# Kernel optimization log

Hardware: AMD Instinct MI355X
Metric: run time of the kernel (lower is better)

The kernel has to match this reference:

```python
import jax, jax.numpy as jnp
import numpy as np

N_SEQ, MAX_LEN, H_DIM, N_CHAR = 8, 4096, 1024, 256


def setup_inputs() -> dict:
    key = jax.random.key(0)
    ks = jax.random.split(key, 10)
    n_char_ev = 32768
    L, E = 12, 16384
    char_i_seq = jax.random.randint(ks[0], (n_char_ev,), 0, N_SEQ)
    char_i_pos = jax.random.randint(ks[1], (n_char_ev,), 0, MAX_LEN)
    char_ids = jax.random.randint(ks[2], (n_char_ev,), 0, N_CHAR)
    grp_i_seq = jax.random.randint(ks[3], (L, E), 0, N_SEQ)
    grp_i_first = jax.random.randint(ks[4], (L, E), 0, MAX_LEN)
    grp_i_second = jax.random.randint(ks[5], (L, E), 0, MAX_LEN)
    grp_i_pos = jax.random.randint(ks[6], (L, E), 0, MAX_LEN)
    # Learned params: embedding table (std = 1/sqrt(h_dim)) and composer Linear(2h -> h)
    emb_char = jax.random.normal(ks[7], (N_CHAR, H_DIM), dtype=jnp.float32) * (1.0 / H_DIM ** 0.5)
    W = jax.random.normal(ks[8], (2 * H_DIM, H_DIM), dtype=jnp.float32) * (1.0 / (2 * H_DIM) ** 0.5)
    b = jnp.zeros((H_DIM,), dtype=jnp.float32)
    return {"char_i_seq": char_i_seq, "char_i_pos": char_i_pos, "char_ids": char_ids,
            "grp_i_seq": grp_i_seq, "grp_i_first": grp_i_first, "grp_i_second": grp_i_second,
            "grp_i_pos": grp_i_pos, "emb_char": emb_char, "W": W, "b": b}


def reference(char_i_seq, char_i_pos, char_ids, grp_i_seq, grp_i_first,
              grp_i_second, grp_i_pos, emb_char, W, b):
    # h_frag: [n_seq, max_len, h_dim]
    h = jnp.zeros((N_SEQ, MAX_LEN, H_DIM), dtype=emb_char.dtype)
    # Leaf characters: embedding lookup + scatter-add
    h = h.at[char_i_seq, char_i_pos].add(emb_char[char_ids])

    def composer(left, right):
        # tanh(Linear(concat(left, right))) : [E, 2h] @ [2h, h] -> [E, h]
        return jnp.tanh(jnp.concatenate([left, right], axis=-1) @ W + b)

    def level_step(h, idx):
        i_seq, i_first, i_second, i_pos = idx
        out = composer(h[i_seq, i_first], h[i_seq, i_second])  # gather -> compose
        return h.at[i_seq, i_pos].add(out), None                # scatter-add

    h, _ = jax.lax.scan(level_step, h, (grp_i_seq, grp_i_first, grp_i_second, grp_i_pos))
    h = h.at[:, 0].set(0.0)  # h_frag[:, 0].fill_(0)
    return h
```

## Files before the change

kernel.cpp:

```cpp
#include <hip/hip_runtime.h>

#define NS 8
#define ML 4096
#define HD 1024
#define K2 2048
#define NEV 32768
#define NLEV 12
#define NE 16384
#define NSLOT (NS * ML)
#define CAP 8
#define BK 64
#define NT (K2 / BK)
#define LDS_BYTES 131072

typedef __attribute__((ext_vector_type(8))) short bf16x8;
typedef __attribute__((ext_vector_type(4))) float f32x4;

typedef __attribute__((address_space(1))) const void cvoid_g;
typedef __attribute__((address_space(3))) void void_l;

static __device__ __forceinline__ void load_lds_16(const void* g, void* l) {
    __builtin_amdgcn_global_load_lds((cvoid_g*)g, (void_l*)l, 16, 0, 0);
}

static __device__ __forceinline__ unsigned short f2bf(float f) {
    unsigned u = __float_as_uint(f);
    unsigned r = (u + 0x7fffu + ((u >> 16) & 1u)) >> 16;
    return (unsigned short)r;
}

static __device__ __forceinline__ float fast_tanh(float x) {
    return 1.0f - 2.0f / (__expf(2.0f * x) + 1.0f);
}

__global__ void wt_kernel(const float* __restrict__ W, unsigned short* __restrict__ WbT) {
    __shared__ unsigned short tile[64][65];
    const int t = threadIdx.x;
    const int k0 = blockIdx.x * 64;
    const int n0 = blockIdx.y * 64;
#pragma unroll
    for (int i = 0; i < 16; i++) {
        int idx = i * 256 + t;
        int r = idx >> 6, c = idx & 63;
        tile[r][c] = f2bf(W[(size_t)(k0 + r) * HD + n0 + c]);
    }
    __syncthreads();
#pragma unroll
    for (int i = 0; i < 16; i++) {
        int idx = i * 256 + t;
        int r = idx >> 6, c = idx & 63;
        WbT[(size_t)(n0 + r) * K2 + k0 + c] = tile[c][r];
    }
}

__global__ void char_ticket(const int* __restrict__ cseq, const int* __restrict__ cpos,
                            int* __restrict__ counts, int* __restrict__ ticket,
                            int* __restrict__ evlist) {
    const int e = blockIdx.x * 256 + threadIdx.x;
    if (e >= NEV) return;
    const int slot = cseq[e] * ML + cpos[e];
    const int t = atomicAdd(&counts[slot], 1);
    ticket[e] = t;
    if (t < CAP) evlist[slot * CAP + t] = e;
}

__global__ void char_slot_sum(const int* __restrict__ counts, const int* __restrict__ evlist,
                              const int* __restrict__ cid, const float* __restrict__ emb,
                              float* __restrict__ h) {
    const int slot = blockIdx.x;
    const int t = threadIdx.x;
    int n = counts[slot];
    if (n > CAP) n = CAP;
    float4 acc = {0.f, 0.f, 0.f, 0.f};
    for (int i = 0; i < n; i++) {
        const int e = evlist[slot * CAP + i];
        const int id = cid[e];
        const float4 v = ((const float4*)(emb + (size_t)id * HD))[t];
        acc.x += v.x; acc.y += v.y; acc.z += v.z; acc.w += v.w;
    }
    ((float4*)(h + (size_t)slot * HD))[t] = acc;
}

__global__ void char_overflow(const int* __restrict__ cseq, const int* __restrict__ cpos,
                              const int* __restrict__ cid, const int* __restrict__ ticket,
                              const float* __restrict__ emb, float* __restrict__ h) {
    const int e0 = blockIdx.x * 128;
    const int t = threadIdx.x;
    for (int i = 0; i < 128; i++) {
        const int e = e0 + i;
        if (ticket[e] < CAP) continue;
        const int slot = cseq[e] * ML + cpos[e];
        const int id = cid[e];
        const float4 v = ((const float4*)(emb + (size_t)id * HD))[t];
        float* dst = h + (size_t)slot * HD + t * 4;
        atomicAdd(dst + 0, v.x);
        atomicAdd(dst + 1, v.y);
        atomicAdd(dst + 2, v.z);
        atomicAdd(dst + 3, v.w);
    }
}

__global__ void grp_count(const int* __restrict__ iseq, const int* __restrict__ ipos,
                          int* __restrict__ gcounts) {
    const int idx = blockIdx.x * 256 + threadIdx.x;
    if (idx >= NLEV * NE) return;
    const int lev = idx >> 14;
    atomicAdd(&gcounts[lev * NSLOT + iseq[idx] * ML + ipos[idx]], 1);
}

__global__ void grp_dup(const int* __restrict__ iseq, const int* __restrict__ ipos,
                        const int* __restrict__ gcounts, unsigned char* __restrict__ dup) {
    const int idx = blockIdx.x * 256 + threadIdx.x;
    if (idx >= NLEV * NE) return;
    const int lev = idx >> 14;
    dup[idx] = (gcounts[lev * NSLOT + iseq[idx] * ML + ipos[idx]] > 1) ? 1 : 0;
}

__global__ void hbf_init(const float* __restrict__ h, unsigned short* __restrict__ hbf) {
    const size_t i = (size_t)blockIdx.x * 256 + threadIdx.x;
    const float4 v = ((const float4*)h)[i];
    ushort4 p;
    p.x = f2bf(v.x); p.y = f2bf(v.y); p.z = f2bf(v.z); p.w = f2bf(v.w);
    ((ushort4*)hbf)[i] = p;
}

__global__ void hbf_refresh(const float* __restrict__ h, const int* __restrict__ iseq,
                            const int* __restrict__ ipos, unsigned short* __restrict__ hbf) {
    const int e = blockIdx.x;
    const int t = threadIdx.x;
    const size_t row = (size_t)iseq[e] * ML + ipos[e];
    const float4 v = ((const float4*)(h + row * HD))[t];
    ushort4 p;
    p.x = f2bf(v.x); p.y = f2bf(v.y); p.z = f2bf(v.z); p.w = f2bf(v.w);
    ((ushort4*)(hbf + row * HD))[t] = p;
}

__global__ __launch_bounds__(512, 2) void gemm_scatter(
    const unsigned short* __restrict__ hbf,
    const unsigned short* __restrict__ WbT,
    const float* __restrict__ bias,
    const int* __restrict__ iseq, const int* __restrict__ ifirst,
    const int* __restrict__ isecond, const int* __restrict__ ipos,
    const unsigned char* __restrict__ dup,
    float* __restrict__ h) {
    extern __shared__ unsigned short lds[];
    const int t = threadIdx.x;
    const int lane = t & 63;
    const int w = t >> 6;
    const int wm = w >> 2;
    const int wn = (w & 3) * 64;
    const int fr = lane & 15, fq = lane >> 4;

    const int bid = blockIdx.x;
    const int xcd = bid & 7, bix = bid >> 3;
    const int row0 = ((xcd & 1) * 32 + bix) * 256;
    const int col0 = (xcd >> 1) * 256;

    const int tr = t >> 3;
    const int sp = (t & 7) ^ (tr & 7);
    unsigned offA0[4], offA1[4];
#pragma unroll
    for (int c = 0; c < 4; c++) {
        const int e = row0 + tr + c * 64;
        const int seq = iseq[e];
        offA0[c] = (unsigned)((seq * ML + ifirst[e]) * HD + sp * 8);
        offA1[c] = (unsigned)((seq * ML + isecond[e]) * HD + sp * 8);
    }
    const unsigned short* Bsrc = WbT + (size_t)(col0 + tr) * K2 + sp * 8;

    f32x4 acc[8][4];
#pragma unroll
    for (int i = 0; i < 8; i++)
#pragma unroll
        for (int j = 0; j < 4; j++) acc[i][j] = (f32x4){0.f, 0.f, 0.f, 0.f};

    {
        unsigned short* dA = lds;
        unsigned short* dB = lds + 16384;
        load_lds_16(Bsrc + (size_t)(0 * 64) * K2, &dB[(0 * 512 + t) * 8]);
        load_lds_16(Bsrc + (size_t)(1 * 64) * K2, &dB[(1 * 512 + t) * 8]);
        load_lds_16(Bsrc + (size_t)(2 * 64) * K2, &dB[(2 * 512 + t) * 8]);
        load_lds_16(Bsrc + (size_t)(3 * 64) * K2, &dB[(3 * 512 + t) * 8]);
        load_lds_16(hbf + offA0[0], &dA[(0 * 512 + t) * 8]);
        load_lds_16(hbf + offA0[2], &dA[(2 * 512 + t) * 8]);
        load_lds_16(hbf + offA0[1], &dA[(1 * 512 + t) * 8]);
        load_lds_16(hbf + offA0[3], &dA[(3 * 512 + t) * 8]);
    }
    asm volatile("s_waitcnt vmcnt(2)\n\ts_barrier" ::: "memory");

    for (int kt = 0; kt < NT; kt++) {
        const int d = kt & 1;
        const unsigned short* sA = lds + d * 32768;
        const unsigned short* sB = sA + 16384;
        unsigned short* nA = lds + (d ^ 1) * 32768;
        unsigned short* nB = nA + 16384;
        const size_t ko = (size_t)(kt + 1) * BK;
        const unsigned koA = (unsigned)(((kt + 1) * BK) & 1023);
        const int hsel = (kt + 1) >= (NT / 2);
        const bool st = (kt + 1 < NT);

        bf16x8 af0[2][4], af1[2][4], bf0[2][2], bf1[2][2];

#pragma unroll
        for (int ks = 0; ks < 2; ks++) {
            const int qs = ((ks * 4 + fq) ^ (fr & 7)) * 8;
#pragma unroll
            for (int mt = 0; mt < 4; mt++)
                af0[ks][mt] = *(const bf16x8*)&sA[(wm * 128 + mt * 16 + fr) * BK + qs];
#pragma unroll
            for (int nt = 0; nt < 2; nt++)
                bf0[ks][nt] = *(const bf16x8*)&sB[(wn + nt * 16 + fr) * BK + qs];
        }
        if (st) {
            load_lds_16(Bsrc + (size_t)(0 * 64) * K2 + ko, &nB[(0 * 512 + t) * 8]);
            load_lds_16(Bsrc + (size_t)(1 * 64) * K2 + ko, &nB[(1 * 512 + t) * 8]);
        }
        asm volatile("s_barrier" ::: "memory");
        __builtin_amdgcn_s_setprio(1);
#pragma unroll
        for (int ks = 0; ks < 2; ks++)
#pragma unroll
            for (int mt = 0; mt < 4; mt++)
#pragma unroll
                for (int nt = 0; nt < 2; nt++)
                    acc[mt][nt] = __builtin_amdgcn_mfma_f32_16x16x32_bf16(
                        af0[ks][mt], bf0[ks][nt], acc[mt][nt], 0, 0, 0);
        __builtin_amdgcn_s_setprio(0);
        asm volatile("s_barrier" ::: "memory");

#pragma unroll
        for (int ks = 0; ks < 2; ks++) {
            const int qs = ((ks * 4 + fq) ^ (fr & 7)) * 8;
#pragma unroll
            for (int nt = 0; nt < 2; nt++)
                bf1[ks][nt] = *(const bf16x8*)&sB[(wn + 32 + nt * 16 + fr) * BK + qs];
        }
        if (st) {
            load_lds_16(Bsrc + (size_t)(2 * 64) * K2 + ko, &nB[(2 * 512 + t) * 8]);
            load_lds_16(Bsrc + (size_t)(3 * 64) * K2 + ko, &nB[(3 * 512 + t) * 8]);
        }
        asm volatile("s_barrier" ::: "memory");
        __builtin_amdgcn_s_setprio(1);
#pragma unroll
        for (int ks = 0; ks < 2; ks++)
#pragma unroll
            for (int mt = 0; mt < 4; mt++)
#pragma unroll
                for (int nt = 0; nt < 2; nt++)
                    acc[mt][2 + nt] = __builtin_amdgcn_mfma_f32_16x16x32_bf16(
                        af0[ks][mt], bf1[ks][nt], acc[mt][2 + nt], 0, 0, 0);
        __builtin_amdgcn_s_setprio(0);
        if (st) { asm volatile("s_waitcnt vmcnt(4)\n\ts_barrier" ::: "memory"); }
        else    { asm volatile("s_waitcnt vmcnt(0)\n\ts_barrier" ::: "memory"); }

#pragma unroll
        for (int ks = 0; ks < 2; ks++) {
            const int qs = ((ks * 4 + fq) ^ (fr & 7)) * 8;
#pragma unroll
            for (int mt = 0; mt < 4; mt++)
                af1[ks][mt] = *(const bf16x8*)&sA[(wm * 128 + 64 + mt * 16 + fr) * BK + qs];
        }
        if (st) {
            const unsigned o0 = (hsel ? offA1[0] : offA0[0]) + koA;
            const unsigned o2 = (hsel ? offA1[2] : offA0[2]) + koA;
            load_lds_16(hbf + o0, &nA[(0 * 512 + t) * 8]);
            load_lds_16(hbf + o2, &nA[(2 * 512 + t) * 8]);
        }
        asm volatile("s_barrier" ::: "memory");
        __builtin_amdgcn_s_setprio(1);
#pragma unroll
        for (int ks = 0; ks < 2; ks++)
#pragma unroll
            for (int mt = 0; mt < 4; mt++)
#pragma unroll
                for (int nt = 0; nt < 2; nt++)
                    acc[4 + mt][nt] = __builtin_amdgcn_mfma_f32_16x16x32_bf16(
                        af1[ks][mt], bf0[ks][nt], acc[4 + mt][nt], 0, 0, 0);
        __builtin_amdgcn_s_setprio(0);
        asm volatile("s_barrier" ::: "memory");

        if (st) {
            const unsigned o1 = (hsel ? offA1[1] : offA0[1]) + koA;
            const unsigned o3 = (hsel ? offA1[3] : offA0[3]) + koA;
            load_lds_16(hbf + o1, &nA[(1 * 512 + t) * 8]);
            load_lds_16(hbf + o3, &nA[(3 * 512 + t) * 8]);
        }
        __builtin_amdgcn_s_setprio(1);
#pragma unroll
        for (int ks = 0; ks < 2; ks++)
#pragma unroll
            for (int mt = 0; mt < 4; mt++)
#pragma unroll
                for (int nt = 0; nt < 2; nt++)
                    acc[4 + mt][2 + nt] = __builtin_amdgcn_mfma_f32_16x16x32_bf16(
                        af1[ks][mt], bf1[ks][nt], acc[4 + mt][2 + nt], 0, 0, 0);
        __builtin_amdgcn_s_setprio(0);
        if (st) { asm volatile("s_waitcnt vmcnt(2)\n\ts_barrier" ::: "memory"); }
        else    { asm volatile("s_waitcnt vmcnt(0)\n\ts_barrier" ::: "memory"); }
    }

    float bv[4];
#pragma unroll
    for (int ni = 0; ni < 4; ni++) bv[ni] = bias[col0 + wn + ni * 16 + fr];
#pragma unroll
    for (int mi = 0; mi < 8; mi++) {
#pragma unroll
        for (int r = 0; r < 4; r++) {
            const int e = row0 + wm * 128 + mi * 16 + fq * 4 + r;
            const int seq = iseq[e], pos = ipos[e];
            float* hrow = h + ((size_t)seq * ML + pos) * HD + col0 + wn;
            if (dup[e]) {
#pragma unroll
                for (int ni = 0; ni < 4; ni++) {
                    float x = fast_tanh(acc[mi][ni][r] + bv[ni]);
                    atomicAdd(&hrow[ni * 16 + fr], x);
                }
            } else {
#pragma unroll
                for (int ni = 0; ni < 4; ni++) {
                    float x = fast_tanh(acc[mi][ni][r] + bv[ni]);
                    hrow[ni * 16 + fr] += x;
                }
            }
        }
    }
}

__global__ void zero_first(float* __restrict__ h) {
    const int t = blockIdx.x * 256 + threadIdx.x;
    const int seq = t >> 10, d = t & 1023;
    h[(size_t)seq * ML * HD + d] = 0.0f;
}

extern "C" void kernel_launch(void* const* d_in, const int* in_sizes, int n_in,
                              void* d_out, int out_size, void* d_ws, size_t ws_size,
                              hipStream_t stream) {
    const int* char_i_seq = (const int*)d_in[0];
    const int* char_i_pos = (const int*)d_in[1];
    const int* char_ids   = (const int*)d_in[2];
    const int* grp_i_seq    = (const int*)d_in[3];
    const int* grp_i_first  = (const int*)d_in[4];
    const int* grp_i_second = (const int*)d_in[5];
    const int* grp_i_pos    = (const int*)d_in[6];
    const float* emb = (const float*)d_in[7];
    const float* W   = (const float*)d_in[8];
    const float* b   = (const float*)d_in[9];
    float* h = (float*)d_out;

    unsigned short* WbT = (unsigned short*)d_ws;
    unsigned short* hbf = (unsigned short*)((char*)d_ws + (8u << 20));
    int* counts = (int*)((char*)d_ws + (72u << 20));
    int* ticket = (int*)((char*)d_ws + (72u << 20) + (1u << 18));
    int* evlist = (int*)((char*)d_ws + (72u << 20) + (1u << 19));
    int* gcounts = (int*)((char*)d_ws + (74u << 20));
    unsigned char* gdup = (unsigned char*)((char*)d_ws + (76u << 20));

    static bool attr_done = false;
    if (!attr_done) {
        (void)hipFuncSetAttribute((const void*)gemm_scatter,
                                  hipFuncAttributeMaxDynamicSharedMemorySize, LDS_BYTES);
        attr_done = true;
    }

    hipMemsetAsync(counts, 0, NSLOT * sizeof(int), stream);
    hipMemsetAsync(gcounts, 0, (size_t)NLEV * NSLOT * sizeof(int), stream);
    wt_kernel<<<dim3(32, 16), 256, 0, stream>>>(W, WbT);
    char_ticket<<<NEV / 256, 256, 0, stream>>>(char_i_seq, char_i_pos, counts, ticket, evlist);
    char_slot_sum<<<NSLOT, 256, 0, stream>>>(counts, evlist, char_ids, emb, h);
    char_overflow<<<NEV / 128, 256, 0, stream>>>(char_i_seq, char_i_pos, char_ids, ticket, emb, h);
    grp_count<<<(NLEV * NE) / 256, 256, 0, stream>>>(grp_i_seq, grp_i_pos, gcounts);
    grp_dup<<<(NLEV * NE) / 256, 256, 0, stream>>>(grp_i_seq, grp_i_pos, gcounts, gdup);
    hbf_init<<<NSLOT, 256, 0, stream>>>(h, hbf);

    for (int lev = 0; lev < NLEV; lev++) {
        const int* iseq = grp_i_seq + lev * NE;
        const int* ifir = grp_i_first + lev * NE;
        const int* isec = grp_i_second + lev * NE;
        const int* ipos = grp_i_pos + lev * NE;
        gemm_scatter<<<dim3(256), 512, LDS_BYTES, stream>>>(hbf, WbT, b, iseq, ifir, isec,
                                                            ipos, gdup + lev * NE, h);
        if (lev + 1 < NLEV)
            hbf_refresh<<<NE, 256, 0, stream>>>(h, iseq, ipos, hbf);
    }
    zero_first<<<32, 256, 0, stream>>>(h);
}
```

Measured before the change: 1.415 ms.

## Load W fragments directly to registers and triple-buffer gathered A in LDS

```diff
diff --git a/kernel.cpp b/kernel.cpp
--- a/kernel.cpp
+++ b/kernel.cpp
@@ -11,7 +11,7 @@
 #define CAP 8
 #define BK 64
 #define NT (K2 / BK)
-#define LDS_BYTES 131072
+#define LDS_BYTES 98304
 
 typedef __attribute__((ext_vector_type(8))) short bf16x8;
 typedef __attribute__((ext_vector_type(4))) float f32x4;
@@ -166,7 +166,13 @@
         offA0[c] = (unsigned)((seq * ML + ifirst[e]) * HD + sp * 8);
         offA1[c] = (unsigned)((seq * ML + isecond[e]) * HD + sp * 8);
     }
-    const unsigned short* Bsrc = WbT + (size_t)(col0 + tr) * K2 + sp * 8;
+
+    unsigned offB[2][4];
+#pragma unroll
+    for (int ks = 0; ks < 2; ks++)
+#pragma unroll
+        for (int nt = 0; nt < 4; nt++)
+            offB[ks][nt] = (unsigned)((col0 + wn + nt * 16 + fr) * K2 + (ks * 4 + fq) * 8);
 
     f32x4 acc[8][4];
 #pragma unroll
@@ -174,33 +180,29 @@
 #pragma unroll
         for (int j = 0; j < 4; j++) acc[i][j] = (f32x4){0.f, 0.f, 0.f, 0.f};
 
+    bf16x8 bfP[2][4], bfQ[2][4];
+
     {
-        unsigned short* dA = lds;
-        unsigned short* dB = lds + 16384;
-        load_lds_16(Bsrc + (size_t)(0 * 64) * K2, &dB[(0 * 512 + t) * 8]);
-        load_lds_16(Bsrc + (size_t)(1 * 64) * K2, &dB[(1 * 512 + t) * 8]);
-        load_lds_16(Bsrc + (size_t)(2 * 64) * K2, &dB[(2 * 512 + t) * 8]);
-        load_lds_16(Bsrc + (size_t)(3 * 64) * K2, &dB[(3 * 512 + t) * 8]);
-        load_lds_16(hbf + offA0[0], &dA[(0 * 512 + t) * 8]);
-        load_lds_16(hbf + offA0[2], &dA[(2 * 512 + t) * 8]);
-        load_lds_16(hbf + offA0[1], &dA[(1 * 512 + t) * 8]);
-        load_lds_16(hbf + offA0[3], &dA[(3 * 512 + t) * 8]);
-    }
-    asm volatile("s_waitcnt vmcnt(2)\n\ts_barrier" ::: "memory");
-
-    for (int kt = 0; kt < NT; kt++) {
-        const int d = kt & 1;
-        const unsigned short* sA = lds + d * 32768;
-        const unsigned short* sB = sA + 16384;
-        unsigned short* nA = lds + (d ^ 1) * 32768;
-        unsigned short* nB = nA + 16384;
-        const size_t ko = (size_t)(kt + 1) * BK;
-        const unsigned koA = (unsigned)(((kt + 1) * BK) & 1023);
-        const int hsel = (kt + 1) >= (NT / 2);
-        const bool st = (kt + 1 < NT);
-
-        bf16x8 af0[2][4], af1[2][4], bf0[2][2], bf1[2][2];
-
+        unsigned short* d0 = lds;
+        unsigned short* d1 = lds + 16384;
+#pragma unroll
+        for (int c = 0; c < 4; c++)
+            load_lds_16(hbf + offA0[c], &d0[(c * 512 + t) * 8]);
+#pragma unroll
+        for (int ks = 0; ks < 2; ks++)
+#pragma unroll
+            for (int nt = 0; nt < 4; nt++)
+                bfP[ks][nt] = *(const bf16x8*)(WbT + offB[ks][nt]);
+#pragma unroll
+        for (int c = 0; c < 4; c++)
+            load_lds_16(hbf + offA0[c] + 64, &d1[(c * 512 + t) * 8]);
+    }
+    asm volatile("s_waitcnt vmcnt(4)\n\ts_barrier" ::: "memory");
+
+    auto body = [&](int kt, bf16x8 (&bfC)[2][4], bf16x8 (&bfN)[2][4]) {
+        const unsigned short* sA = lds + (kt % 3) * 16384;
+
+        bf16x8 af0[2][4], af1[2][4];
 #pragma unroll
         for (int ks = 0; ks < 2; ks++) {
             const int qs = ((ks * 4 + fq) ^ (fr & 7)) * 8;
@@ -208,95 +210,58 @@
             for (int mt = 0; mt < 4; mt++)
                 af0[ks][mt] = *(const bf16x8*)&sA[(wm * 128 + mt * 16 + fr) * BK + qs];
 #pragma unroll
-            for (int nt = 0; nt < 2; nt++)
-                bf0[ks][nt] = *(const bf16x8*)&sB[(wn + nt * 16 + fr) * BK + qs];
-        }
-        if (st) {
-            load_lds_16(Bsrc + (size_t)(0 * 64) * K2 + ko, &nB[(0 * 512 + t) * 8]);
-            load_lds_16(Bsrc + (size_t)(1 * 64) * K2 + ko, &nB[(1 * 512 + t) * 8]);
-        }
-        asm volatile("s_barrier" ::: "memory");
-        __builtin_amdgcn_s_setprio(1);
-#pragma unroll
-        for (int ks = 0; ks < 2; ks++)
-#pragma unroll
-            for (int mt = 0; mt < 4; mt++)
-#pragma unroll
-                for (int nt = 0; nt < 2; nt++)
-                    acc[mt][nt] = __builtin_amdgcn_mfma_f32_16x16x32_bf16(
-                        af0[ks][mt], bf0[ks][nt], acc[mt][nt], 0, 0, 0);
-        __builtin_amdgcn_s_setprio(0);
-        asm volatile("s_barrier" ::: "memory");
-
-#pragma unroll
-        for (int ks = 0; ks < 2; ks++) {
-            const int qs = ((ks * 4 + fq) ^ (fr & 7)) * 8;
-#pragma unroll
-            for (int nt = 0; nt < 2; nt++)
-                bf1[ks][nt] = *(const bf16x8*)&sB[(wn + 32 + nt * 16 + fr) * BK + qs];
-        }
-        if (st) {
-            load_lds_16(Bsrc + (size_t)(2 * 64) * K2 + ko, &nB[(2 * 512 + t) * 8]);
-            load_lds_16(Bsrc + (size_t)(3 * 64) * K2 + ko, &nB[(3 * 512 + t) * 8]);
-        }
-        asm volatile("s_barrier" ::: "memory");
-        __builtin_amdgcn_s_setprio(1);
-#pragma unroll
-        for (int ks = 0; ks < 2; ks++)
-#pragma unroll
-            for (int mt = 0; mt < 4; mt++)
-#pragma unroll
-                for (int nt = 0; nt < 2; nt++)
-                    acc[mt][2 + nt] = __builtin_amdgcn_mfma_f32_16x16x32_bf16(
-                        af0[ks][mt], bf1[ks][nt], acc[mt][2 + nt], 0, 0, 0);
-        __builtin_amdgcn_s_setprio(0);
-        if (st) { asm volatile("s_waitcnt vmcnt(4)\n\ts_barrier" ::: "memory"); }
-        else    { asm volatile("s_waitcnt vmcnt(0)\n\ts_barrier" ::: "memory"); }
-
-#pragma unroll
-        for (int ks = 0; ks < 2; ks++) {
-            const int qs = ((ks * 4 + fq) ^ (fr & 7)) * 8;
-#pragma unroll
             for (int mt = 0; mt < 4; mt++)
                 af1[ks][mt] = *(const bf16x8*)&sA[(wm * 128 + 64 + mt * 16 + fr) * BK + qs];
         }
-        if (st) {
-            const unsigned o0 = (hsel ? offA1[0] : offA0[0]) + koA;
-            const unsigned o2 = (hsel ? offA1[2] : offA0[2]) + koA;
-            load_lds_16(hbf + o0, &nA[(0 * 512 + t) * 8]);
-            load_lds_16(hbf + o2, &nA[(2 * 512 + t) * 8]);
-        }
-        asm volatile("s_barrier" ::: "memory");
+
+        if (kt + 1 < NT) {
+            const unsigned kb = (unsigned)((kt + 1) * BK);
+#pragma unroll
+            for (int ks = 0; ks < 2; ks++)
+#pragma unroll
+                for (int nt = 0; nt < 4; nt++)
+                    bfN[ks][nt] = *(const bf16x8*)(WbT + offB[ks][nt] + kb);
+        }
+
+        if (kt + 2 < NT) {
+            unsigned short* nA = lds + ((kt + 2) % 3) * 16384;
+            const unsigned koA = (unsigned)(((kt + 2) * BK) & 1023);
+            const int hsel = (kt + 2) >= (NT / 2);
+#pragma unroll
+            for (int c = 0; c < 4; c++) {
+                const unsigned o = (hsel ? offA1[c] : offA0[c]) + koA;
+                load_lds_16(hbf + o, &nA[(c * 512 + t) * 8]);
+            }
+        }
+
         __builtin_amdgcn_s_setprio(1);
 #pragma unroll
         for (int ks = 0; ks < 2; ks++)
 #pragma unroll
             for (int mt = 0; mt < 4; mt++)
 #pragma unroll
-                for (int nt = 0; nt < 2; nt++)
+                for (int nt = 0; nt < 4; nt++)
+                    acc[mt][nt] = __builtin_amdgcn_mfma_f32_16x16x32_bf16(
+                        af0[ks][mt], bfC[ks][nt], acc[mt][nt], 0, 0, 0);
+#pragma unroll
+        for (int ks = 0; ks < 2; ks++)
+#pragma unroll
+            for (int mt = 0; mt < 4; mt++)
+#pragma unroll
+                for (int nt = 0; nt < 4; nt++)
                     acc[4 + mt][nt] = __builtin_amdgcn_mfma_f32_16x16x32_bf16(
-                        af1[ks][mt], bf0[ks][nt], acc[4 + mt][nt], 0, 0, 0);
+                        af1[ks][mt], bfC[ks][nt], acc[4 + mt][nt], 0, 0, 0);
         __builtin_amdgcn_s_setprio(0);
-        asm volatile("s_barrier" ::: "memory");
-
-        if (st) {
-            const unsigned o1 = (hsel ? offA1[1] : offA0[1]) + koA;
-            const unsigned o3 = (hsel ? offA1[3] : offA0[3]) + koA;
-            load_lds_16(hbf + o1, &nA[(1 * 512 + t) * 8]);
-            load_lds_16(hbf + o3, &nA[(3 * 512 + t) * 8]);
-        }
-        __builtin_amdgcn_s_setprio(1);
-#pragma unroll
-        for (int ks = 0; ks < 2; ks++)
-#pragma unroll
-            for (int mt = 0; mt < 4; mt++)
-#pragma unroll
-                for (int nt = 0; nt < 2; nt++)
-                    acc[4 + mt][2 + nt] = __builtin_amdgcn_mfma_f32_16x16x32_bf16(
-                        af1[ks][mt], bf1[ks][nt], acc[4 + mt][2 + nt], 0, 0, 0);
-        __builtin_amdgcn_s_setprio(0);
-        if (st) { asm volatile("s_waitcnt vmcnt(2)\n\ts_barrier" ::: "memory"); }
-        else    { asm volatile("s_waitcnt vmcnt(0)\n\ts_barrier" ::: "memory"); }
+
+        if (kt + 1 < NT) {
+            if (kt + 2 < NT) { asm volatile("s_waitcnt vmcnt(4)\n\ts_barrier" ::: "memory"); }
+            else             { asm volatile("s_waitcnt vmcnt(0)\n\ts_barrier" ::: "memory"); }
+        }
+    };
+
+    for (int kt = 0; kt < NT; kt += 2) {
+        body(kt, bfP, bfQ);
+        body(kt + 1, bfQ, bfP);
     }
 
     float bv[4];
```

Measured after the change: 4.774 ms. +237.5%, slower.
